# Performance work log

Hardware: AMD Instinct MI355X
Metric: run time of the kernel (lower is better)

The kernel has to match this reference:

```python
import jax, jax.numpy as jnp
import numpy as np

N = 50000   # num_node
E = 1600000 # edge_size (N * avg_degree 32)
B = 64      # batch, hardcoded via repeat(64,1,1) in the torch module


def setup_inputs() -> dict:
    key = jax.random.key(0)
    k = jax.random.split(key, 8)
    return {
        "t": jax.random.normal(k[0], (1,), dtype=jnp.float32),
        "input": jax.random.normal(k[1], (B, N), dtype=jnp.float32),
        "edge_i": jax.random.randint(k[2], (E,), 0, N, dtype=jnp.int32),
        "edge_j": jax.random.randint(k[3], (E,), 0, N, dtype=jnp.int32),
        "weight_react": jax.random.normal(k[4], (1, E), dtype=jnp.float32) / 10.0,
        "weight_diff": jax.random.normal(k[5], (1, E), dtype=jnp.float32) / 1000.0,
        "bias_reaction": jax.random.normal(k[6], (1, N), dtype=jnp.float32) / 10.0,
        "bias_diffusion": jax.random.normal(k[7], (1, N), dtype=jnp.float32) / 10.0,
    }


def _lap_matvec(x, w, src, dst, n):
    # W[src_e, dst_e] = w_e (duplicates coalesce by sum, as torch sparse_coo_tensor does)
    # L = diag(colsum(W)) - W ; returns x @ L^T applied batched: out[b, v] = (L x[b])[v]
    col = jax.ops.segment_sum(w, dst, num_segments=n)                 # [N] column sums
    msg = jax.ops.segment_sum(w[:, None] * x[:, dst].T, src,
                              num_segments=n)                          # [N, B]
    return col[None, :] * x - msg.T                                   # [B, N]


def reference(t, input, edge_i, edge_j, weight_react, weight_diff,
              bias_reaction, bias_diffusion):
    x = input                                                          # [B, N]
    n = x.shape[1]
    # reaction Laplacian uses edges (i -> j); diffusion uses transposed (j -> i)
    reaction = _lap_matvec(x, weight_react[0], edge_i, edge_j, n) + bias_reaction
    diffusion = _lap_matvec(x, weight_diff[0], edge_j, edge_i, n) + bias_diffusion
    # up and down both True: tanh(reaction) + diffusion + input
    return jnp.tanh(reaction) + diffusion + x
```

## Files before the change

kernel.cpp:

```cpp
#include <hip/hip_runtime.h>
#include <hip/hip_fp16.h>


#define BKT_SHIFT 7
#define BKT_NODES 128
#define RCAP 4608
#define RCAP2 5504
#define CH 4096
#define NBP 512

#define RFL(x) __builtin_amdgcn_readfirstlane(x)

__device__ __forceinline__ unsigned bf16_rne(float f) {
    unsigned u = __float_as_uint(f);
    unsigned rb = (u >> 16) & 1u;
    u += 0x7FFFu + rb;
    return u >> 16;
}
__device__ __forceinline__ float bf16_lo(int y) {
    return __uint_as_float(((unsigned)y) << 16);
}
__device__ __forceinline__ float bf16_hi(int y) {
    return __uint_as_float((unsigned)y & 0xFFFF0000u);
}

__global__ void transpose_kernel(const float* __restrict__ x, __half* __restrict__ xth,
                                 int* __restrict__ gcur, int ngcur, int N) {
    __shared__ float tile[64][65];
    int v0 = blockIdx.x * 64;
    int tx = threadIdx.x;
    int ty = threadIdx.y;
    int flat = blockIdx.x * 1024 + ty * 64 + tx;
    if (flat < ngcur) gcur[flat] = 0;
    if (v0 + tx < N) {
        for (int b = ty; b < 64; b += 16)
            tile[tx][b] = x[b * N + v0 + tx];
    }
    __syncthreads();
    for (int vl = ty; vl < 64; vl += 16) {
        int v = v0 + vl;
        if (v < N)
            xth[(size_t)v * 64 + tx] = __float2half(tile[vl][tx]);
    }
}

__global__ void __launch_bounds__(512) partition_kernel(
        const int* __restrict__ ei, const int* __restrict__ ej,
        const float* __restrict__ wr, const float* __restrict__ wd,
        int* __restrict__ gcur, int2* __restrict__ runs,
        int E, int NB) {
    __shared__ int cnt[2 * NBP];
    __shared__ int base_a[2 * NBP];
    __shared__ int gb[2 * NBP];
    __shared__ int2 buf[2 * CH];

    int tid = threadIdx.x;
    int e0 = blockIdx.x * CH;
    int ch_len = min(CH, E - e0);
    if (ch_len <= 0) return;

    int my_i[8], my_j[8];
    unsigned my_w[8];
    #pragma unroll
    for (int k = 0; k < 8; ++k) {
        int t = tid + k * 512;
        if (t < ch_len) {
            int e = e0 + t;
            my_i[k] = ei[e];
            my_j[k] = ej[e];
            my_w[k] = (bf16_rne(wr[e]) << 16) | bf16_rne(wd[e]);
        } else {
            my_i[k] = -1;
        }
    }

    for (int b = tid; b < 2 * NBP; b += 512) cnt[b] = 0;
    __syncthreads();
    #pragma unroll
    for (int k = 0; k < 8; ++k) {
        if (my_i[k] >= 0) {
            atomicAdd(&cnt[my_i[k] >> BKT_SHIFT], 1);
            atomicAdd(&cnt[NBP + (my_j[k] >> BKT_SHIFT)], 1);
        }
    }
    __syncthreads();
    if (tid < 64) {
        int carry = 0;
        #pragma unroll
        for (int c = 0; c < (2 * NBP) / 64; ++c) {
            int idx = c * 64 + tid;
            int val = cnt[idx];
            int scan = val;
            for (int off = 1; off < 64; off <<= 1) {
                int n = __shfl_up(scan, off, 64);
                if (tid >= off) scan += n;
            }
            int excl = scan - val + carry;
            base_a[idx] = excl;
            cnt[idx] = excl;
            carry += __shfl(scan, 63, 64);
        }
    }
    __syncthreads();
    #pragma unroll
    for (int k = 0; k < 8; ++k) {
        if (my_i[k] >= 0) {
            int i = my_i[k], j = my_j[k];
            unsigned wv = my_w[k];
            int b0 = i >> BKT_SHIFT;
            int p0 = atomicAdd(&cnt[b0], 1);
            buf[p0] = make_int2((int)(((unsigned)b0 << 23) | ((unsigned)(i & 127) << 16) | (unsigned)j),
                                (int)wv);
            int b1 = j >> BKT_SHIFT;
            int p1 = atomicAdd(&cnt[NBP + b1], 1);
            buf[p1] = make_int2((int)(((unsigned)b1 << 23) | ((unsigned)(j & 127) << 16) | (unsigned)i),
                                (int)((wv << 16) | (wv >> 16)));
        }
    }
    __syncthreads();
    for (int cb = tid; cb < 2 * NBP; cb += 512) {
        int n = cnt[cb] - base_a[cb];
        if (n > 0) {
            int side = cb >> 9;
            int bkt = cb & (NBP - 1);
            gb[cb] = atomicAdd(&gcur[side * NB + bkt], n);
        }
    }
    __syncthreads();
    int total = 2 * ch_len;
    for (int t = tid; t < total; t += 512) {
        int2 p = buf[t];
        int side = (t >= ch_len) ? 1 : 0;
        int bkt = ((unsigned)p.x >> 23) & 0x1FF;
        int cb = side * NBP + bkt;
        int rank = gb[cb] + (t - base_a[cb]);
        if (rank < RCAP)
            runs[((size_t)(side * NB + bkt)) * RCAP + rank] = p;
    }
}

#define ACC8(P, D)                                                        \
    {                                                                     \
        float wv_ = bf16_hi(P);                                           \
        float2 f_;                                                        \
        f_ = __half22float2(*(const __half2*)&(D).x);                     \
        a0 = fmaf(wv_, f_.x, a0); a1 = fmaf(wv_, f_.y, a1);               \
        f_ = __half22float2(*(const __half2*)&(D).y);                     \
        a2 = fmaf(wv_, f_.x, a2); a3 = fmaf(wv_, f_.y, a3);               \
        f_ = __half22float2(*(const __half2*)&(D).z);                     \
        a4 = fmaf(wv_, f_.x, a4); a5 = fmaf(wv_, f_.y, a5);               \
        f_ = __half22float2(*(const __half2*)&(D).w);                     \
        a6 = fmaf(wv_, f_.x, a6); a7 = fmaf(wv_, f_.y, a7);               \
    }

#define COMB3(A) { A += __shfl_xor(A, 8); A += __shfl_xor(A, 16); A += __shfl_xor(A, 32); }

__global__ void __launch_bounds__(512) sortgather_kernel(
        const int* __restrict__ gcur, const int2* __restrict__ runs,
        const __half* __restrict__ xth,
        __half* __restrict__ msg, float* __restrict__ colsum,
        int NB, int N) {
    __shared__ int cnt[BKT_NODES];
    __shared__ int cur[BKT_NODES];
    __shared__ int pb[BKT_NODES];
    __shared__ float csum[BKT_NODES];
    __shared__ int dst[RCAP2];

    int sb = blockIdx.x;
    int side = (sb >= NB) ? 1 : 0;
    int b = sb - side * NB;
    int v0 = b << BKT_SHIFT;
    int len = min(gcur[sb], RCAP);
    size_t roff = (size_t)sb * RCAP;
    int tid = threadIdx.x;

    int2 my[9];
    #pragma unroll
    for (int k = 0; k < 9; ++k) {
        int t = tid + k * 512;
        if (t < len) my[k] = runs[roff + t];
        else my[k].x = -1;
    }

    if (tid < BKT_NODES) { cnt[tid] = 0; csum[tid] = 0.f; }
    __syncthreads();
    #pragma unroll
    for (int k = 0; k < 9; ++k) {
        if (my[k].x != -1) {
            int dl = ((unsigned)my[k].x >> 16) & 0x7F;
            atomicAdd(&cnt[dl], 1);
            atomicAdd(&csum[dl], bf16_lo(my[k].y));
        }
    }
    __syncthreads();
    if (tid < 64) {
        int carry = 0;
        #pragma unroll
        for (int c = 0; c < BKT_NODES / 64; ++c) {
            int idx = c * 64 + tid;
            int val = (cnt[idx] + 7) & ~7;
            int scan = val;
            for (int off = 1; off < 64; off <<= 1) {
                int n = __shfl_up(scan, off, 64);
                if (tid >= off) scan += n;
            }
            int excl = scan - val + carry;
            pb[idx] = excl;
            cur[idx] = excl;
            carry += __shfl(scan, 63, 64);
        }
    }
    __syncthreads();
    if (tid < BKT_NODES) {
        int pc = (cnt[tid] + 7) & ~7;
        for (int t = cnt[tid]; t < pc; ++t) dst[pb[tid] + t] = 0;
    }
    __syncthreads();
    #pragma unroll
    for (int k = 0; k < 9; ++k) {
        if (my[k].x != -1) {
            int dl = ((unsigned)my[k].x >> 16) & 0x7F;
            int pos = atomicAdd(&cur[dl], 1);
            dst[pos] = (int)(((unsigned)my[k].y & 0xFFFF0000u) | ((unsigned)my[k].x & 0xFFFFu));
        }
    }
    __syncthreads();

    const uint4* __restrict__ xq = (const uint4*)xth;
    int lane = tid & 63;
    int g  = lane >> 3;
    int bl = lane & 7;
    int wid = tid >> 6;
    for (int t = 0; t < BKT_NODES / 8; ++t) {
        int dl = wid * (BKT_NODES / 8) + t;
        int v = v0 + dl;
        if (v >= N) continue;
        const int* pay = dst + pb[dl] + g;
        int noct = ((cnt[dl] + 7) & ~7) >> 3;
        float a0 = 0.f, a1 = 0.f, a2 = 0.f, a3 = 0.f;
        float a4 = 0.f, a5 = 0.f, a6 = 0.f, a7 = 0.f;
        int o = 0;
        for (; o + 4 <= noct; o += 4) {
            int pA = pay[8 * o];
            int pB = pay[8 * o + 8];
            int pC = pay[8 * o + 16];
            int pD = pay[8 * o + 24];
            uint4 dA = xq[(((size_t)((unsigned)pA & 0xFFFFu)) << 3) + bl];
            uint4 dB = xq[(((size_t)((unsigned)pB & 0xFFFFu)) << 3) + bl];
            uint4 dC = xq[(((size_t)((unsigned)pC & 0xFFFFu)) << 3) + bl];
            uint4 dD = xq[(((size_t)((unsigned)pD & 0xFFFFu)) << 3) + bl];
            ACC8(pA, dA)
            ACC8(pB, dB)
            ACC8(pC, dC)
            ACC8(pD, dD)
        }
        for (; o < noct; ++o) {
            int p = pay[8 * o];
            uint4 d = xq[(((size_t)((unsigned)p & 0xFFFFu)) << 3) + bl];
            ACC8(p, d)
        }
        COMB3(a0) COMB3(a1) COMB3(a2) COMB3(a3)
        COMB3(a4) COMB3(a5) COMB3(a6) COMB3(a7)
        if (lane < 8) {
            __half2 h0 = __floats2half2_rn(a0, a1);
            __half2 h1 = __floats2half2_rn(a2, a3);
            __half2 h2 = __floats2half2_rn(a4, a5);
            __half2 h3 = __floats2half2_rn(a6, a7);
            uint4 st = make_uint4(*(unsigned*)&h0, *(unsigned*)&h1,
                                  *(unsigned*)&h2, *(unsigned*)&h3);
            *(uint4*)(msg + ((size_t)side * N + v) * 64 + 8 * lane) = st;
        }
        if (lane == 0)
            colsum[(size_t)side * N + v] = csum[dl];
    }
}

__global__ void final_kernel(const float* __restrict__ x,
                             const __half* __restrict__ msg,
                             const float* __restrict__ colsum,
                             const float* __restrict__ br, const float* __restrict__ bd,
                             float* __restrict__ out, int N) {
    __shared__ float tr[64][65];
    __shared__ float td[64][65];
    int v0 = blockIdx.x * 64;
    int tx = threadIdx.x;
    int ty = threadIdx.y;
    for (int vl = ty; vl < 64; vl += 16) {
        int v = v0 + vl;
        if (v < N) {
            tr[vl][tx] = __half2float(msg[(size_t)v * 64 + tx]);
            td[vl][tx] = __half2float(msg[((size_t)N + v) * 64 + tx]);
        }
    }
    __syncthreads();
    int v = v0 + tx;
    if (v < N) {
        float cold = colsum[v];
        float colr = colsum[(size_t)N + v];
        float brv = br[v], bdv = bd[v];
        for (int b = ty; b < 64; b += 16) {
            float xv = x[b * N + v];
            float r = colr * xv - tr[tx][b] + brv;
            float d = cold * xv - td[tx][b] + bdv;
            out[b * N + v] = tanhf(r) + d + xv;
        }
    }
}

extern "C" void kernel_launch(void* const* d_in, const int* in_sizes, int n_in,
                              void* d_out, int out_size, void* d_ws, size_t ws_size,
                              hipStream_t stream) {
    const float* x  = (const float*)d_in[1];
    const int*   ei = (const int*)d_in[2];
    const int*   ej = (const int*)d_in[3];
    const float* wr = (const float*)d_in[4];
    const float* wd = (const float*)d_in[5];
    const float* br = (const float*)d_in[6];
    const float* bd = (const float*)d_in[7];
    float* out = (float*)d_out;

    int E = in_sizes[2];
    int N = in_sizes[6];
    int NB = (N + BKT_NODES - 1) >> BKT_SHIFT;
    (void)out_size; (void)ws_size; (void)n_in;

    char* w = (char*)d_ws;
    __half* xth = (__half*)w;    w += (size_t)N * 64 * 2;
    __half* msg = (__half*)w;    w += (size_t)2 * N * 64 * 2;
    float* colsum = (float*)w;   w += (size_t)2 * N * 4;
    int* gcur   = (int*)w;       w += (size_t)2 * NB * 4;
    w = (char*)(((uintptr_t)w + 15) & ~(uintptr_t)15);
    int2* runs  = (int2*)w;

    dim3 tb(64, 16);
    int ntiles = (N + 63) / 64;
    transpose_kernel<<<ntiles, tb, 0, stream>>>(x, xth, gcur, 2 * NB, N);

    int nchunks = (E + CH - 1) / CH;
    partition_kernel<<<nchunks, 512, 0, stream>>>(ei, ej, wr, wd, gcur, runs, E, NB);

    sortgather_kernel<<<2 * NB, 512, 0, stream>>>(gcur, runs, xth, msg, colsum, NB, N);

    final_kernel<<<ntiles, tb, 0, stream>>>(x, msg, colsum, br, bd, out, N);
}
```

Before: 205.0 us.

## Split gather kernel into two batch-half passes to shrink per-pass gather footprint

The sort-and-gather kernel now runs twice, and each launch handles 32 of the 64 batch columns with 8-byte gathers instead of 16-byte ones. Each pass touches only half of the transposed x table, which is meant to improve cache hit rates for the random gathers. The cost is that the per-bucket local sort (loading runs, counting, scanning, scattering into shared memory) is done twice, along with an extra launch. The column sum is computed only in the first pass.

```diff
diff --git a/kernel.cpp b/kernel.cpp
--- a/kernel.cpp
+++ b/kernel.cpp
@@ -139,7 +139,7 @@
     }
 }
 
-#define ACC8(P, D)                                                        \
+#define ACC4(P, D)                                                        \
     {                                                                     \
         float wv_ = bf16_hi(P);                                           \
         float2 f_;                                                        \
@@ -147,10 +147,6 @@
         a0 = fmaf(wv_, f_.x, a0); a1 = fmaf(wv_, f_.y, a1);               \
         f_ = __half22float2(*(const __half2*)&(D).y);                     \
         a2 = fmaf(wv_, f_.x, a2); a3 = fmaf(wv_, f_.y, a3);               \
-        f_ = __half22float2(*(const __half2*)&(D).z);                     \
-        a4 = fmaf(wv_, f_.x, a4); a5 = fmaf(wv_, f_.y, a5);               \
-        f_ = __half22float2(*(const __half2*)&(D).w);                     \
-        a6 = fmaf(wv_, f_.x, a6); a7 = fmaf(wv_, f_.y, a7);               \
     }
 
 #define COMB3(A) { A += __shfl_xor(A, 8); A += __shfl_xor(A, 16); A += __shfl_xor(A, 32); }
@@ -159,7 +155,7 @@
         const int* __restrict__ gcur, const int2* __restrict__ runs,
         const __half* __restrict__ xth,
         __half* __restrict__ msg, float* __restrict__ colsum,
-        int NB, int N) {
+        int NB, int N, int h) {
     __shared__ int cnt[BKT_NODES];
     __shared__ int cur[BKT_NODES];
     __shared__ int pb[BKT_NODES];
@@ -189,7 +185,7 @@
         if (my[k].x != -1) {
             int dl = ((unsigned)my[k].x >> 16) & 0x7F;
             atomicAdd(&cnt[dl], 1);
-            atomicAdd(&csum[dl], bf16_lo(my[k].y));
+            if (h == 0) atomicAdd(&csum[dl], bf16_lo(my[k].y));
         }
     }
     __syncthreads();
@@ -226,10 +222,11 @@
     }
     __syncthreads();
 
-    const uint4* __restrict__ xq = (const uint4*)xth;
+    const uint2* __restrict__ xq = (const uint2*)xth;
     int lane = tid & 63;
     int g  = lane >> 3;
     int bl = lane & 7;
+    int hb = h * 8 + (lane & 7);
     int wid = tid >> 6;
     for (int t = 0; t < BKT_NODES / 8; ++t) {
         int dl = wid * (BKT_NODES / 8) + t;
@@ -238,39 +235,34 @@
         const int* pay = dst + pb[dl] + g;
         int noct = ((cnt[dl] + 7) & ~7) >> 3;
         float a0 = 0.f, a1 = 0.f, a2 = 0.f, a3 = 0.f;
-        float a4 = 0.f, a5 = 0.f, a6 = 0.f, a7 = 0.f;
         int o = 0;
         for (; o + 4 <= noct; o += 4) {
             int pA = pay[8 * o];
             int pB = pay[8 * o + 8];
             int pC = pay[8 * o + 16];
             int pD = pay[8 * o + 24];
-            uint4 dA = xq[(((size_t)((unsigned)pA & 0xFFFFu)) << 3) + bl];
-            uint4 dB = xq[(((size_t)((unsigned)pB & 0xFFFFu)) << 3) + bl];
-            uint4 dC = xq[(((size_t)((unsigned)pC & 0xFFFFu)) << 3) + bl];
-            uint4 dD = xq[(((size_t)((unsigned)pD & 0xFFFFu)) << 3) + bl];
-            ACC8(pA, dA)
-            ACC8(pB, dB)
-            ACC8(pC, dC)
-            ACC8(pD, dD)
+            uint2 dA = xq[(((size_t)((unsigned)pA & 0xFFFFu)) << 4) + hb];
+            uint2 dB = xq[(((size_t)((unsigned)pB & 0xFFFFu)) << 4) + hb];
+            uint2 dC = xq[(((size_t)((unsigned)pC & 0xFFFFu)) << 4) + hb];
+            uint2 dD = xq[(((size_t)((unsigned)pD & 0xFFFFu)) << 4) + hb];
+            ACC4(pA, dA)
+            ACC4(pB, dB)
+            ACC4(pC, dC)
+            ACC4(pD, dD)
         }
         for (; o < noct; ++o) {
             int p = pay[8 * o];
-            uint4 d = xq[(((size_t)((unsigned)p & 0xFFFFu)) << 3) + bl];
-            ACC8(p, d)
+            uint2 d = xq[(((size_t)((unsigned)p & 0xFFFFu)) << 4) + hb];
+            ACC4(p, d)
         }
         COMB3(a0) COMB3(a1) COMB3(a2) COMB3(a3)
-        COMB3(a4) COMB3(a5) COMB3(a6) COMB3(a7)
         if (lane < 8) {
             __half2 h0 = __floats2half2_rn(a0, a1);
             __half2 h1 = __floats2half2_rn(a2, a3);
-            __half2 h2 = __floats2half2_rn(a4, a5);
-            __half2 h3 = __floats2half2_rn(a6, a7);
-            uint4 st = make_uint4(*(unsigned*)&h0, *(unsigned*)&h1,
-                                  *(unsigned*)&h2, *(unsigned*)&h3);
-            *(uint4*)(msg + ((size_t)side * N + v) * 64 + 8 * lane) = st;
-        }
-        if (lane == 0)
+            uint2 st = make_uint2(*(unsigned*)&h0, *(unsigned*)&h1);
+            *(uint2*)(msg + ((size_t)side * N + v) * 64 + h * 32 + 4 * lane) = st;
+        }
+        if (h == 0 && lane == 0)
             colsum[(size_t)side * N + v] = csum[dl];
     }
 }
@@ -339,7 +331,8 @@
     int nchunks = (E + CH - 1) / CH;
     partition_kernel<<<nchunks, 512, 0, stream>>>(ei, ej, wr, wd, gcur, runs, E, NB);
 
-    sortgather_kernel<<<2 * NB, 512, 0, stream>>>(gcur, runs, xth, msg, colsum, NB, N);
+    sortgather_kernel<<<2 * NB, 512, 0, stream>>>(gcur, runs, xth, msg, colsum, NB, N, 0);
+    sortgather_kernel<<<2 * NB, 512, 0, stream>>>(gcur, runs, xth, msg, colsum, NB, N, 1);
 
     final_kernel<<<ntiles, tb, 0, stream>>>(x, msg, colsum, br, bd, out, N);
 }
```

Result: slower. 227.3 us (+10.9%).

## Compute per-node counts and column sums with global atomics in partition

Applied to the files above, without the earlier changes.

Moves the per-node edge counting and column-sum accumulation out of the sortgather kernel into the partition kernel, using global atomics on new cnt_node and colsum arrays. These arrays are zeroed by the transpose kernel. This removes the shared-memory atomic histogram pass in sortgather, but adds four global atomics per edge, about 6.4M in total, spread over 100k addresses each. The column sums are now accumulated in fp32 from the raw weights instead of the bf16-rounded ones.

```diff
diff --git a/kernel.cpp b/kernel.cpp
--- a/kernel.cpp
+++ b/kernel.cpp
@@ -9,29 +9,24 @@
 #define CH 4096
 #define NBP 512
 
-#define RFL(x) __builtin_amdgcn_readfirstlane(x)
-
 __device__ __forceinline__ unsigned bf16_rne(float f) {
     unsigned u = __float_as_uint(f);
     unsigned rb = (u >> 16) & 1u;
     u += 0x7FFFu + rb;
     return u >> 16;
 }
-__device__ __forceinline__ float bf16_lo(int y) {
-    return __uint_as_float(((unsigned)y) << 16);
-}
 __device__ __forceinline__ float bf16_hi(int y) {
     return __uint_as_float((unsigned)y & 0xFFFF0000u);
 }
 
 __global__ void transpose_kernel(const float* __restrict__ x, __half* __restrict__ xth,
-                                 int* __restrict__ gcur, int ngcur, int N) {
+                                 int* __restrict__ zbuf, int nz, int N) {
     __shared__ float tile[64][65];
     int v0 = blockIdx.x * 64;
     int tx = threadIdx.x;
     int ty = threadIdx.y;
     int flat = blockIdx.x * 1024 + ty * 64 + tx;
-    if (flat < ngcur) gcur[flat] = 0;
+    if (flat < nz) zbuf[flat] = 0;
     if (v0 + tx < N) {
         for (int b = ty; b < 64; b += 16)
             tile[tx][b] = x[b * N + v0 + tx];
@@ -48,7 +43,8 @@
         const int* __restrict__ ei, const int* __restrict__ ej,
         const float* __restrict__ wr, const float* __restrict__ wd,
         int* __restrict__ gcur, int2* __restrict__ runs,
-        int E, int NB) {
+        int* __restrict__ cnt_node, float* __restrict__ colsum,
+        int E, int NB, int N) {
     __shared__ int cnt[2 * NBP];
     __shared__ int base_a[2 * NBP];
     __shared__ int gb[2 * NBP];
@@ -66,9 +62,15 @@
         int t = tid + k * 512;
         if (t < ch_len) {
             int e = e0 + t;
-            my_i[k] = ei[e];
-            my_j[k] = ej[e];
-            my_w[k] = (bf16_rne(wr[e]) << 16) | bf16_rne(wd[e]);
+            int iv = ei[e], jv = ej[e];
+            float wrv = wr[e], wdv = wd[e];
+            my_i[k] = iv;
+            my_j[k] = jv;
+            my_w[k] = (bf16_rne(wrv) << 16) | bf16_rne(wdv);
+            atomicAdd(&cnt_node[iv], 1);
+            atomicAdd(&cnt_node[N + jv], 1);
+            atomicAdd(&colsum[iv], wdv);
+            atomicAdd(&colsum[N + jv], wrv);
         } else {
             my_i[k] = -1;
         }
@@ -157,13 +159,12 @@
 
 __global__ void __launch_bounds__(512) sortgather_kernel(
         const int* __restrict__ gcur, const int2* __restrict__ runs,
-        const __half* __restrict__ xth,
-        __half* __restrict__ msg, float* __restrict__ colsum,
+        const int* __restrict__ cnt_node,
+        const __half* __restrict__ xth, __half* __restrict__ msg,
         int NB, int N) {
     __shared__ int cnt[BKT_NODES];
     __shared__ int cur[BKT_NODES];
     __shared__ int pb[BKT_NODES];
-    __shared__ float csum[BKT_NODES];
     __shared__ int dst[RCAP2];
 
     int sb = blockIdx.x;
@@ -182,15 +183,9 @@
         else my[k].x = -1;
     }
 
-    if (tid < BKT_NODES) { cnt[tid] = 0; csum[tid] = 0.f; }
-    __syncthreads();
-    #pragma unroll
-    for (int k = 0; k < 9; ++k) {
-        if (my[k].x != -1) {
-            int dl = ((unsigned)my[k].x >> 16) & 0x7F;
-            atomicAdd(&cnt[dl], 1);
-            atomicAdd(&csum[dl], bf16_lo(my[k].y));
-        }
+    if (tid < BKT_NODES) {
+        int v = v0 + tid;
+        cnt[tid] = (v < N) ? cnt_node[side * N + v] : 0;
     }
     __syncthreads();
     if (tid < 64) {
@@ -270,8 +265,6 @@
                                   *(unsigned*)&h2, *(unsigned*)&h3);
             *(uint4*)(msg + ((size_t)side * N + v) * 64 + 8 * lane) = st;
         }
-        if (lane == 0)
-            colsum[(size_t)side * N + v] = csum[dl];
     }
 }
 
@@ -328,18 +321,23 @@
     __half* xth = (__half*)w;    w += (size_t)N * 64 * 2;
     __half* msg = (__half*)w;    w += (size_t)2 * N * 64 * 2;
     float* colsum = (float*)w;   w += (size_t)2 * N * 4;
+    int* cnt_node = (int*)w;     w += (size_t)2 * N * 4;
     int* gcur   = (int*)w;       w += (size_t)2 * NB * 4;
     w = (char*)(((uintptr_t)w + 15) & ~(uintptr_t)15);
     int2* runs  = (int2*)w;
 
+    int nz = 4 * N + 2 * NB;
+
     dim3 tb(64, 16);
     int ntiles = (N + 63) / 64;
-    transpose_kernel<<<ntiles, tb, 0, stream>>>(x, xth, gcur, 2 * NB, N);
+    transpose_kernel<<<ntiles, tb, 0, stream>>>(x, xth, (int*)colsum, nz, N);
 
     int nchunks = (E + CH - 1) / CH;
-    partition_kernel<<<nchunks, 512, 0, stream>>>(ei, ej, wr, wd, gcur, runs, E, NB);
-
-    sortgather_kernel<<<2 * NB, 512, 0, stream>>>(gcur, runs, xth, msg, colsum, NB, N);
+    partition_kernel<<<nchunks, 512, 0, stream>>>(ei, ej, wr, wd, gcur, runs,
+                                                  cnt_node, colsum, E, NB, N);
+
+    sortgather_kernel<<<2 * NB, 512, 0, stream>>>(gcur, runs, cnt_node, xth,
+                                                  msg, NB, N);
 
     final_kernel<<<ntiles, tb, 0, stream>>>(x, msg, colsum, br, bd, out, N);
 }
```

New measurement: 449.9 us. 2.19x slower.
